# Kernel tuning notes

Hardware: AMD Instinct MI355X
Metric: run time of the kernel (lower is better)

Reference implementation:

```python
import jax, jax.numpy as jnp
import numpy as np

N, C, K2 = 40000, 128, 9  # active voxels, channels, 3x3 kernel taps
HEAD_OUT = {"hm": 3, "center": 2, "center_z": 1, "dim": 3, "rot": 2}
EPS = 1e-5
INIT_BIAS = -2.66


def setup_inputs() -> dict:
    key = jax.random.key(0)
    ks = jax.random.split(key, 16)
    feats = jax.random.normal(ks[0], (N, C), dtype=jnp.float32)
    # precomputed submanifold-conv neighbor indices (one per kernel tap, all valid)
    nbr_idx = jax.random.randint(ks[1], (N, K2), 0, N, dtype=jnp.int32)
    H = len(HEAD_OUT)
    inp = {"feats": feats, "nbr_idx": nbr_idx}
    # stacked 3x3 SubMConv weights for all heads (kaiming-ish scale)
    inp["W1"] = jax.random.normal(ks[2], (H, K2, C, C), dtype=jnp.float32) * (2.0 / (K2 * C)) ** 0.5
    inp["gamma"] = jnp.ones((H, C), jnp.float32)
    inp["beta"] = jnp.zeros((H, C), jnp.float32)
    for i, (name, oc) in enumerate(HEAD_OUT.items()):
        inp[f"w_{name}"] = jax.random.normal(ks[3 + i], (C, oc), dtype=jnp.float32) * (2.0 / C) ** 0.5
        inp[f"b_{name}"] = (jnp.full((oc,), INIT_BIAS, jnp.float32) if name == "hm"
                             else jnp.zeros((oc,), jnp.float32))
    return inp


def reference(feats, nbr_idx, W1, gamma, beta,
              w_hm, b_hm, w_center, b_center, w_center_z, b_center_z,
              w_dim, b_dim, w_rot, b_rot):
    # SubMConv2d as gather + contraction over kernel taps (shared by all heads)
    gathered = feats[nbr_idx]                       # [N, K2, C]
    y = jnp.einsum('nkc,hkcd->hnd', gathered, W1)   # [H, N, C]
    # BatchNorm1d (training-mode forward: biased batch stats over voxels) + ReLU
    mean = y.mean(axis=1, keepdims=True)
    var = y.var(axis=1, keepdims=True)
    y = jax.nn.relu((y - mean) * jax.lax.rsqrt(var + EPS) * gamma[:, None, :] + beta[:, None, :])
    # per-head 1x1 SubMConv with bias
    heads = [(w_hm, b_hm), (w_center, b_center), (w_center_z, b_center_z),
             (w_dim, b_dim), (w_rot, b_rot)]
    outs = [y[i] @ w + b for i, (w, b) in enumerate(heads)]
    # concat head outputs along channel: [N, 3+2+1+3+2] = [N, 11]
    return jnp.concatenate(outs, axis=-1)
```

## Files before the change

kernel.cpp:

```cpp
#include <hip/hip_runtime.h>
#include <stdint.h>

#define NVOX 40000
#define CCH  128
#define K2   9
#define NH   5
#define TILES 313

typedef __attribute__((ext_vector_type(8))) short bf16x8;
typedef __attribute__((ext_vector_type(4))) float f32x4;

__device__ __forceinline__ unsigned short f2b(float f) {
  union { float f; unsigned int u; } v; v.f = f;
  return (unsigned short)((v.u + 0x7fffu + ((v.u >> 16) & 1u)) >> 16);
}
__device__ __forceinline__ float b2f(unsigned short u) {
  union { unsigned int u; float f; } v; v.u = ((unsigned int)u) << 16;
  return v.f;
}
__device__ __forceinline__ void g2l16(const void* g, void* l) {
  __builtin_amdgcn_global_load_lds(
      (const __attribute__((address_space(1))) unsigned int*)g,
      (__attribute__((address_space(3))) unsigned int*)l, 16, 0, 0);
}
__device__ __forceinline__ int swz(int row, int col) {
  return row * 128 + ((((col >> 3) ^ (row & 15)) << 3) | (col & 7));
}

__global__ void prep(const float4* __restrict__ feats, ushort4* __restrict__ fb,
                     const float* __restrict__ w1, unsigned short* __restrict__ w1t,
                     float* __restrict__ sums) {
  __shared__ unsigned short t[128 * 34];
  int b = blockIdx.x;
  if (b < 5000) {
    int i = b * 256 + threadIdx.x;
    if (i < NVOX * CCH / 4) {
      float4 v = feats[i];
      ushort4 r;
      r.x = f2b(v.x); r.y = f2b(v.y); r.z = f2b(v.z); r.w = f2b(v.w);
      fb[i] = r;
    }
    return;
  }
  if (b == 5180) {
    for (int i = threadIdx.x; i < 2 * NH * CCH; i += 256) sums[i] = 0.f;
    return;
  }
  int bb = b - 5000;
  int tile = bb >> 2;
  int q = bb & 3;
  const float* src = w1 + (size_t)tile * 16384 + q * 32 * 128;
  for (int e = threadIdx.x; e < 4096; e += 256) {
    int c = e >> 7, d = e & 127;
    t[d * 34 + c] = f2b(src[e]);
  }
  __syncthreads();
  unsigned short* dst = w1t + (size_t)tile * 16384 + q * 32;
  for (int e = threadIdx.x; e < 4096; e += 256) {
    int d = e >> 5, c = e & 31;
    dst[d * 128 + c] = t[d * 34 + c];
  }
}

__device__ __forceinline__ void stageB(unsigned short* dstbuf, const unsigned short* wp,
                                       int wave, int lane) {
  int lcol = lane & 15, lrow = lane >> 4;
#pragma unroll
  for (int i = 0; i < 8; ++i) {
    int elem = wave * 4096 + i * 512;
    int row = (elem >> 7) + lrow;
    g2l16(wp + row * 128 + ((lcol ^ (row & 15)) << 3), &dstbuf[elem]);
  }
}

__device__ __forceinline__ void stageA(unsigned short* dstbuf, const unsigned short* fb,
                                       const int* idxs, int k, int wave, int lane) {
  int lcol = lane & 15, lrow = lane >> 4;
  int ridx[8];
#pragma unroll
  for (int i = 0; i < 8; ++i)
    ridx[i] = idxs[(wave * 32 + i * 4 + lrow) * K2 + k];
#pragma unroll
  for (int i = 0; i < 8; ++i) {
    int row = wave * 32 + i * 4 + lrow;
    g2l16(fb + (size_t)ridx[i] * CCH + ((lcol ^ (row & 15)) << 3),
          &dstbuf[(wave * 32 + i * 4) * CCH]);
  }
}

__global__ void __launch_bounds__(256, 1) conv_gemm(
    const unsigned short* __restrict__ fb,
    const int* __restrict__ nbr,
    const unsigned short* __restrict__ w1t,
    unsigned short* __restrict__ yb,
    float* __restrict__ sums)
{
  __shared__ __align__(16) unsigned short Asb[2][128 * 128];
  __shared__ __align__(16) unsigned short Bsb[2][128 * 128];
  __shared__ int idxs[128 * K2];

  const int bid = blockIdx.x;
  const int s = bid / 40;
  const int r = bid % 40;
  const int h = r >> 3;
  const int x = r & 7;
  const int tile = s * 8 + x;
  if (tile >= TILES) return;
  const int n0 = tile * 128;

  const int tid = threadIdx.x;
  const int wave = tid >> 6;
  const int lane = tid & 63;
  const int lcol = lane & 15;
  const int lrow = lane >> 4;
  const int wm = wave >> 1, wn = wave & 1;

  stageB(Bsb[0], w1t + (((size_t)h * K2) << 14), wave, lane);

  for (int i = tid; i < 128 * K2; i += 256) {
    int rr = i / K2;
    int gn = n0 + rr; if (gn > NVOX - 1) gn = NVOX - 1;
    idxs[i] = nbr[gn * K2 + (i - rr * K2)];
  }
  __syncthreads();
  stageA(Asb[0], fb, idxs, 0, wave, lane);
  asm volatile("s_waitcnt vmcnt(0)" ::: "memory");
  __syncthreads();

  f32x4 acc[4][4] = {};

  for (int k = 0; k < K2; ++k) {
    const int buf = k & 1;
    if (k + 1 < K2) {
      stageA(Asb[buf ^ 1], fb, idxs, k + 1, wave, lane);
      stageB(Bsb[buf ^ 1], w1t + (((size_t)h * K2 + k + 1) << 14), wave, lane);
    }
    const unsigned short* Acur = Asb[buf];
    const unsigned short* Bcur = Bsb[buf];

#pragma unroll
    for (int kc = 0; kc < 4; ++kc) {
      bf16x8 af[4], bfr[4];
#pragma unroll
      for (int mi = 0; mi < 4; ++mi) {
        int row = wm * 64 + mi * 16 + lcol;
        af[mi] = *(const bf16x8*)&Acur[row * CCH + (((kc * 4 + lrow) ^ (row & 15)) << 3)];
      }
#pragma unroll
      for (int ni = 0; ni < 4; ++ni) {
        int row = wn * 64 + ni * 16 + lcol;
        bfr[ni] = *(const bf16x8*)&Bcur[row * CCH + (((kc * 4 + lrow) ^ (row & 15)) << 3)];
      }
#pragma unroll
      for (int mi = 0; mi < 4; ++mi)
#pragma unroll
        for (int ni = 0; ni < 4; ++ni)
          acc[mi][ni] = __builtin_amdgcn_mfma_f32_16x16x32_bf16(af[mi], bfr[ni], acc[mi][ni], 0, 0, 0);
    }

    if (k + 1 < K2) {
      asm volatile("s_waitcnt vmcnt(0)" ::: "memory");
      __syncthreads();
    }
  }

  const bool full = (n0 + 128 <= NVOX);

  unsigned short* epi = Asb[1];
#pragma unroll
  for (int mi = 0; mi < 4; ++mi)
#pragma unroll
    for (int ni = 0; ni < 4; ++ni)
#pragma unroll
      for (int rr = 0; rr < 4; ++rr) {
        int row = wm * 64 + mi * 16 + lrow * 4 + rr;
        int col = wn * 64 + ni * 16 + lcol;
        epi[swz(row, col)] = f2b(acc[mi][ni][rr]);
      }

  float2* pb = (float2*)Bsb[1];
#pragma unroll
  for (int ni = 0; ni < 4; ++ni) {
    float sm = 0.f, q = 0.f;
#pragma unroll
    for (int mi = 0; mi < 4; ++mi)
#pragma unroll
      for (int rr = 0; rr < 4; ++rr) {
        float v = acc[mi][ni][rr];
        if (!full && n0 + wm * 64 + mi * 16 + lrow * 4 + rr >= NVOX) v = 0.f;
        sm += v; q += v * v;
      }
    pb[(wn * 64 + ni * 16 + lcol) * 9 + wm * 4 + lrow] = make_float2(sm, q);
  }
  __syncthreads();

  for (int i = tid; i < 2048; i += 256) {
    int row = i >> 4;
    int c = i & 15;
    if (n0 + row < NVOX)
      *(bf16x8*)(yb + ((size_t)h * NVOX + n0 + row) * CCH + c * 8) =
          *(const bf16x8*)&epi[row * 128 + ((c ^ (row & 15)) << 3)];
  }

  if (tid < 128) {
    float sm = 0.f, q = 0.f;
#pragma unroll
    for (int c = 0; c < 8; ++c) {
      float2 p = pb[tid * 9 + c];
      sm += p.x; q += p.y;
    }
    atomicAdd(&sums[h * CCH + tid], sm);
    atomicAdd(&sums[NH * CCH + h * CCH + tid], q);
  }
}

__global__ void finalize_bn(const float* __restrict__ sums, const float* __restrict__ gamma,
                            const float* __restrict__ beta, float* __restrict__ ssb) {
  int h = blockIdx.x, c = threadIdx.x;
  float mean = sums[h * CCH + c] * (1.f / NVOX);
  float var = sums[NH * CCH + h * CCH + c] * (1.f / NVOX) - mean * mean;
  float rstd = rsqrtf(var + 1e-5f);
  float scale = rstd * gamma[h * CCH + c];
  ssb[h * CCH + c] = scale;
  ssb[NH * CCH + h * CCH + c] = beta[h * CCH + c] - mean * scale;
}

__global__ void __launch_bounds__(256) head_fuse(
    const unsigned short* __restrict__ yb, const float* __restrict__ ssb,
    const float* __restrict__ w_hm, const float* __restrict__ b_hm,
    const float* __restrict__ w_ce, const float* __restrict__ b_ce,
    const float* __restrict__ w_cz, const float* __restrict__ b_cz,
    const float* __restrict__ w_dm, const float* __restrict__ b_dm,
    const float* __restrict__ w_rt, const float* __restrict__ b_rt,
    float* __restrict__ out)
{
  __shared__ unsigned short t[64 * 128];
  __shared__ float pbuf[4][64][12];

  const int tid = threadIdx.x;
  const int v0 = blockIdx.x * 64;
  const int vx = tid & 63;
  const int qd = tid >> 6;

  float part[11];
#pragma unroll
  for (int j = 0; j < 11; ++j) part[j] = 0.f;

#pragma unroll
  for (int h = 0; h < NH; ++h) {
    __syncthreads();
#pragma unroll
    for (int i = 0; i < 4; ++i) {
      int idx = i * 256 + tid;
      int row = idx >> 4, c = idx & 15;
      *(bf16x8*)&t[row * 128 + ((c ^ (row & 15)) << 3)] =
          *(const bf16x8*)(yb + ((size_t)h * NVOX + v0 + row) * CCH + c * 8);
    }
    __syncthreads();

    const float* sc = ssb + h * CCH;
    const float* sh = ssb + NH * CCH + h * CCH;
    const float* wp; int oc, off;
    switch (h) {
      case 0: wp = w_hm; oc = 3; off = 0; break;
      case 1: wp = w_ce; oc = 2; off = 3; break;
      case 2: wp = w_cz; oc = 1; off = 5; break;
      case 3: wp = w_dm; oc = 3; off = 6; break;
      default: wp = w_rt; oc = 2; off = 9; break;
    }
#pragma unroll
    for (int qq = 0; qq < 4; ++qq) {
      int q8 = qd * 4 + qq;
      bf16x8 pk = *(const bf16x8*)&t[vx * 128 + ((q8 ^ (vx & 15)) << 3)];
#pragma unroll
      for (int e = 0; e < 8; ++e) {
        int d = q8 * 8 + e;
        float z = fmaf(b2f((unsigned short)pk[e]), sc[d], sh[d]);
        z = fmaxf(z, 0.f);
        const float* wr = wp + d * oc;
        part[off] = fmaf(z, wr[0], part[off]);
        if (oc > 1) part[off + 1] = fmaf(z, wr[1], part[off + 1]);
        if (oc > 2) part[off + 2] = fmaf(z, wr[2], part[off + 2]);
      }
    }
  }

#pragma unroll
  for (int j = 0; j < 11; ++j) pbuf[qd][vx][j] = part[j];
  __syncthreads();
  if (tid < 64) {
    float o[11];
#pragma unroll
    for (int j = 0; j < 11; ++j)
      o[j] = pbuf[0][tid][j] + pbuf[1][tid][j] + pbuf[2][tid][j] + pbuf[3][tid][j];
    o[0] += b_hm[0]; o[1] += b_hm[1]; o[2] += b_hm[2];
    o[3] += b_ce[0]; o[4] += b_ce[1];
    o[5] += b_cz[0];
    o[6] += b_dm[0]; o[7] += b_dm[1]; o[8] += b_dm[2];
    o[9] += b_rt[0]; o[10] += b_rt[1];
    float* op = out + (size_t)(v0 + tid) * 11;
#pragma unroll
    for (int j = 0; j < 11; ++j) op[j] = o[j];
  }
}

extern "C" void kernel_launch(void* const* d_in, const int* in_sizes, int n_in,
                              void* d_out, int out_size, void* d_ws, size_t ws_size,
                              hipStream_t stream) {
  const float* feats = (const float*)d_in[0];
  const int*   nbr   = (const int*)d_in[1];
  const float* W1    = (const float*)d_in[2];
  const float* gamma = (const float*)d_in[3];
  const float* beta  = (const float*)d_in[4];
  const float* w_hm = (const float*)d_in[5];  const float* b_hm = (const float*)d_in[6];
  const float* w_ce = (const float*)d_in[7];  const float* b_ce = (const float*)d_in[8];
  const float* w_cz = (const float*)d_in[9];  const float* b_cz = (const float*)d_in[10];
  const float* w_dm = (const float*)d_in[11]; const float* b_dm = (const float*)d_in[12];
  const float* w_rt = (const float*)d_in[13]; const float* b_rt = (const float*)d_in[14];
  float* out = (float*)d_out;

  char* ws = (char*)d_ws;
  unsigned short* w1t = (unsigned short*)ws;
  unsigned short* fb  = (unsigned short*)(ws + 11796480);
  unsigned short* yb  = (unsigned short*)(ws + 22036480);
  float* sums = (float*)(ws + 73236480);
  float* ssb  = (float*)(ws + 73241600);

  prep<<<5181, 256, 0, stream>>>((const float4*)feats, (ushort4*)fb, W1, w1t, sums);
  conv_gemm<<<1600, 256, 0, stream>>>(fb, nbr, w1t, yb, sums);
  finalize_bn<<<NH, CCH, 0, stream>>>(sums, gamma, beta, ssb);
  head_fuse<<<625, 256, 0, stream>>>(yb, ssb, w_hm, b_hm, w_ce, b_ce, w_cz, b_cz,
                                     w_dm, b_dm, w_rt, b_rt, out);
}
```

Measured before the change: 277.7 us.

## Load gathered A fragments directly into registers and drop A shared buffer

The gathered feature rows now go straight from global memory into MFMA register fragments, double-buffered across kernel taps, so the A tile no longer passes through LDS. The warp layout changes so each wave owns 32 rows and all 128 output columns, reading B fragments from LDS. Halving LDS use and raising launch bounds to 2 blocks per CU is meant to improve occupancy and hide gather latency. The cost is more VGPRs per thread, uncoalesced 16-byte global loads per lane, and more B reads from LDS per wave.

Result: faster. 237.1 us (-14.6%).

```diff
diff --git a/kernel.cpp b/kernel.cpp
--- a/kernel.cpp
+++ b/kernel.cpp
@@ -73,29 +73,13 @@
   }
 }
 
-__device__ __forceinline__ void stageA(unsigned short* dstbuf, const unsigned short* fb,
-                                       const int* idxs, int k, int wave, int lane) {
-  int lcol = lane & 15, lrow = lane >> 4;
-  int ridx[8];
-#pragma unroll
-  for (int i = 0; i < 8; ++i)
-    ridx[i] = idxs[(wave * 32 + i * 4 + lrow) * K2 + k];
-#pragma unroll
-  for (int i = 0; i < 8; ++i) {
-    int row = wave * 32 + i * 4 + lrow;
-    g2l16(fb + (size_t)ridx[i] * CCH + ((lcol ^ (row & 15)) << 3),
-          &dstbuf[(wave * 32 + i * 4) * CCH]);
-  }
-}
-
-__global__ void __launch_bounds__(256, 1) conv_gemm(
+__global__ void __launch_bounds__(256, 2) conv_gemm(
     const unsigned short* __restrict__ fb,
     const int* __restrict__ nbr,
     const unsigned short* __restrict__ w1t,
     unsigned short* __restrict__ yb,
     float* __restrict__ sums)
 {
-  __shared__ __align__(16) unsigned short Asb[2][128 * 128];
   __shared__ __align__(16) unsigned short Bsb[2][128 * 128];
   __shared__ int idxs[128 * K2];
 
@@ -111,11 +95,12 @@
   const int tid = threadIdx.x;
   const int wave = tid >> 6;
   const int lane = tid & 63;
-  const int lcol = lane & 15;
-  const int lrow = lane >> 4;
-  const int wm = wave >> 1, wn = wave & 1;
-
-  stageB(Bsb[0], w1t + (((size_t)h * K2) << 14), wave, lane);
+  const int m = lane & 15;
+  const int quad = lane >> 4;
+
+  const unsigned short* wh = w1t + ((size_t)h * K2 << 14);
+
+  stageB(Bsb[0], wh, wave, lane);
 
   for (int i = tid; i < 128 * K2; i += 256) {
     int rr = i / K2;
@@ -123,74 +108,84 @@
     idxs[i] = nbr[gn * K2 + (i - rr * K2)];
   }
   __syncthreads();
-  stageA(Asb[0], fb, idxs, 0, wave, lane);
-  asm volatile("s_waitcnt vmcnt(0)" ::: "memory");
-  __syncthreads();
-
-  f32x4 acc[4][4] = {};
-
+
+  bf16x8 A[2][2][4];
+  {
+    int i0 = idxs[(wave * 32 + m) * K2 + 0];
+    int i1 = idxs[(wave * 32 + 16 + m) * K2 + 0];
+    const unsigned short* p0 = fb + (size_t)i0 * CCH + quad * 8;
+    const unsigned short* p1 = fb + (size_t)i1 * CCH + quad * 8;
+#pragma unroll
+    for (int kc = 0; kc < 4; ++kc) {
+      A[0][0][kc] = *(const bf16x8*)(p0 + kc * 32);
+      A[0][1][kc] = *(const bf16x8*)(p1 + kc * 32);
+    }
+  }
+
+  f32x4 acc[2][8] = {};
+
+#pragma unroll
   for (int k = 0; k < K2; ++k) {
-    const int buf = k & 1;
+    const int par = k & 1;
     if (k + 1 < K2) {
-      stageA(Asb[buf ^ 1], fb, idxs, k + 1, wave, lane);
-      stageB(Bsb[buf ^ 1], w1t + (((size_t)h * K2 + k + 1) << 14), wave, lane);
-    }
-    const unsigned short* Acur = Asb[buf];
-    const unsigned short* Bcur = Bsb[buf];
-
+      stageB(Bsb[par ^ 1], wh + ((size_t)(k + 1) << 14), wave, lane);
+      int i0 = idxs[(wave * 32 + m) * K2 + k + 1];
+      int i1 = idxs[(wave * 32 + 16 + m) * K2 + k + 1];
+      const unsigned short* p0 = fb + (size_t)i0 * CCH + quad * 8;
+      const unsigned short* p1 = fb + (size_t)i1 * CCH + quad * 8;
+#pragma unroll
+      for (int kc = 0; kc < 4; ++kc) {
+        A[par ^ 1][0][kc] = *(const bf16x8*)(p0 + kc * 32);
+        A[par ^ 1][1][kc] = *(const bf16x8*)(p1 + kc * 32);
+      }
+    }
+    const unsigned short* Bcur = Bsb[par];
 #pragma unroll
     for (int kc = 0; kc < 4; ++kc) {
-      bf16x8 af[4], bfr[4];
-#pragma unroll
-      for (int mi = 0; mi < 4; ++mi) {
-        int row = wm * 64 + mi * 16 + lcol;
-        af[mi] = *(const bf16x8*)&Acur[row * CCH + (((kc * 4 + lrow) ^ (row & 15)) << 3)];
-      }
-#pragma unroll
-      for (int ni = 0; ni < 4; ++ni) {
-        int row = wn * 64 + ni * 16 + lcol;
-        bfr[ni] = *(const bf16x8*)&Bcur[row * CCH + (((kc * 4 + lrow) ^ (row & 15)) << 3)];
-      }
-#pragma unroll
-      for (int mi = 0; mi < 4; ++mi)
-#pragma unroll
-        for (int ni = 0; ni < 4; ++ni)
-          acc[mi][ni] = __builtin_amdgcn_mfma_f32_16x16x32_bf16(af[mi], bfr[ni], acc[mi][ni], 0, 0, 0);
-    }
-
+      bf16x8 bfr[8];
+#pragma unroll
+      for (int ni = 0; ni < 8; ++ni)
+        bfr[ni] = *(const bf16x8*)&Bcur[(ni * 16 + m) * CCH + (((kc * 4 + quad) ^ m) << 3)];
+#pragma unroll
+      for (int ni = 0; ni < 8; ++ni) {
+        acc[0][ni] = __builtin_amdgcn_mfma_f32_16x16x32_bf16(A[par][0][kc], bfr[ni], acc[0][ni], 0, 0, 0);
+        acc[1][ni] = __builtin_amdgcn_mfma_f32_16x16x32_bf16(A[par][1][kc], bfr[ni], acc[1][ni], 0, 0, 0);
+      }
+    }
     if (k + 1 < K2) {
       asm volatile("s_waitcnt vmcnt(0)" ::: "memory");
       __syncthreads();
     }
   }
 
+  __syncthreads();
   const bool full = (n0 + 128 <= NVOX);
-
-  unsigned short* epi = Asb[1];
-#pragma unroll
-  for (int mi = 0; mi < 4; ++mi)
-#pragma unroll
-    for (int ni = 0; ni < 4; ++ni)
+  unsigned short* epi = (unsigned short*)Bsb[0];
+  float2* pb = (float2*)Bsb[1];
+
+#pragma unroll
+  for (int mi = 0; mi < 2; ++mi)
+#pragma unroll
+    for (int ni = 0; ni < 8; ++ni)
 #pragma unroll
       for (int rr = 0; rr < 4; ++rr) {
-        int row = wm * 64 + mi * 16 + lrow * 4 + rr;
-        int col = wn * 64 + ni * 16 + lcol;
+        int row = wave * 32 + mi * 16 + quad * 4 + rr;
+        int col = ni * 16 + m;
         epi[swz(row, col)] = f2b(acc[mi][ni][rr]);
       }
 
-  float2* pb = (float2*)Bsb[1];
-#pragma unroll
-  for (int ni = 0; ni < 4; ++ni) {
+#pragma unroll
+  for (int ni = 0; ni < 8; ++ni) {
     float sm = 0.f, q = 0.f;
 #pragma unroll
-    for (int mi = 0; mi < 4; ++mi)
+    for (int mi = 0; mi < 2; ++mi)
 #pragma unroll
       for (int rr = 0; rr < 4; ++rr) {
         float v = acc[mi][ni][rr];
-        if (!full && n0 + wm * 64 + mi * 16 + lrow * 4 + rr >= NVOX) v = 0.f;
+        if (!full && n0 + wave * 32 + mi * 16 + quad * 4 + rr >= NVOX) v = 0.f;
         sm += v; q += v * v;
       }
-    pb[(wn * 64 + ni * 16 + lcol) * 9 + wm * 4 + lrow] = make_float2(sm, q);
+    pb[(ni * 16 + m) * 17 + wave * 4 + quad] = make_float2(sm, q);
   }
   __syncthreads();
 
@@ -205,8 +200,8 @@
   if (tid < 128) {
     float sm = 0.f, q = 0.f;
 #pragma unroll
-    for (int c = 0; c < 8; ++c) {
-      float2 p = pb[tid * 9 + c];
+    for (int c = 0; c < 16; ++c) {
+      float2 p = pb[tid * 17 + c];
       sm += p.x; q += p.y;
     }
     atomicAdd(&sums[h * CCH + tid], sm);
```
